# Optimization experiments

Hardware: AMD Instinct MI355X
Metric: run time of the kernel (lower is better)

The kernel has to match this reference:

```python
import jax, jax.numpy as jnp
import numpy as np

EPS = 0.05    # geomloss: blur**p with p=1, blur=0.05
NITER = 30    # fixed Sinkhorn iterations (geomloss uses eps-scaling; fixed-eps loop is the reference math)


def _cost(x, y):
    # x:(N,3), y:(M,3) -> (N,M) Euclidean distance (p=1 ground cost)
    d2 = jnp.sum((x[:, None, :] - y[None, :, :]) ** 2, axis=-1)
    return jnp.sqrt(d2 + 1e-12)


def _sinkhorn_ot(x, y):
    # Entropic OT cost between uniform measures on x (N pts) and y (M pts), log-domain Sinkhorn.
    n, m = x.shape[0], y.shape[0]
    C = _cost(x, y)                                  # (N,M)
    log_a = jnp.full((n,), -jnp.log(jnp.float32(n)), dtype=x.dtype)
    log_b = jnp.full((m,), -jnp.log(jnp.float32(m)), dtype=x.dtype)

    def step(carry, _):
        f, g = carry
        # f_i = -eps * LSE_j( log_b_j + (g_j - C_ij)/eps )
        f = -EPS * jax.nn.logsumexp(log_b[None, :] + (g[None, :] - C) / EPS, axis=1)
        g = -EPS * jax.nn.logsumexp(log_a[:, None] + (f[:, None] - C) / EPS, axis=0)
        return (f, g), None

    f0 = jnp.zeros((n,), dtype=x.dtype)
    g0 = jnp.zeros((m,), dtype=x.dtype)
    (f, g), _ = jax.lax.scan(step, (f0, g0), None, length=NITER)
    a = jnp.exp(log_a)
    b = jnp.exp(log_b)
    return jnp.sum(a * f) + jnp.sum(b * g)


def _sinkhorn_divergence(x, y):
    # Debiased Sinkhorn divergence: S(x,y) = OT(x,y) - 0.5*OT(x,x) - 0.5*OT(y,y)
    return _sinkhorn_ot(x, y) - 0.5 * _sinkhorn_ot(x, x) - 0.5 * _sinkhorn_ot(y, y)


def setup_inputs() -> dict:
    key = jax.random.key(0)
    k1, k2 = jax.random.split(key)
    B, N, M = 8, 2048, 2048
    xyz1 = jax.random.normal(k1, (B, N, 3), dtype=jnp.float32)
    xyz2 = jax.random.normal(k2, (B, M, 3), dtype=jnp.float32)
    return {"xyz1": xyz1, "xyz2": xyz2}


def reference(xyz1, xyz2):
    # Per-batch Sinkhorn divergence, averaged over batch (original loops over b; vmap is the
    # vectorized equivalent since clouds are independent).
    losses = jax.vmap(_sinkhorn_divergence)(xyz1, xyz2)   # (B,)
    return jnp.sum(losses) / xyz1.shape[0]
```

## Files before the change

kernel.cpp:

```cpp
#include <hip/hip_runtime.h>

#define NPTS    2048
#define NBATCH  8
#define NPROB   24
#define NITER   30
#define TPB     512
#define WPB     8
#define NJOBS   32
#define HCOLS   1024
#define CPW     128

constexpr float KSC = 28.853900817779268f;
constexpr float C1f = 0.38123094930796995f;
constexpr float C2f = 0.03465735902799726f;

typedef float v2f __attribute__((ext_vector_type(2)));

__device__ __forceinline__ float fexp2(float x) { return __builtin_amdgcn_exp2f(x); }
__device__ __forceinline__ float flog2(float x) { return __builtin_amdgcn_logf(x); }
__device__ __forceinline__ float fsqrt(float x) { return __builtin_amdgcn_sqrtf(x); }

__global__ __launch_bounds__(256)
void init_sums(float* __restrict__ gsum)
{
    int i = blockIdx.x * 256 + threadIdx.x;
    if (i < NPROB * 2 * NPTS) gsum[i] = 1024.0f;
}

__device__ __forceinline__ void problem_barrier(unsigned* arrive, unsigned* epoch,
                                                unsigned phase, int nbpp, int tid)
{
    __syncthreads();
    if (tid == 0) {
        unsigned old = __hip_atomic_fetch_add(arrive, 1u, __ATOMIC_ACQ_REL,
                                              __HIP_MEMORY_SCOPE_AGENT);
        if (old == (unsigned)(nbpp - 1)) {
            __hip_atomic_store(arrive, 0u, __ATOMIC_RELAXED, __HIP_MEMORY_SCOPE_AGENT);
            __hip_atomic_store(epoch, phase, __ATOMIC_RELEASE, __HIP_MEMORY_SCOPE_AGENT);
        } else {
            while (__hip_atomic_load(epoch, __ATOMIC_RELAXED,
                                     __HIP_MEMORY_SCOPE_AGENT) < phase) {
                __builtin_amdgcn_s_sleep(2);
            }
            __threadfence();
        }
    }
    __syncthreads();
}

__global__ __launch_bounds__(TPB, 6)
void sinkhorn_all(const float* __restrict__ xyz1,
                  const float* __restrict__ xyz2,
                  float* __restrict__ fsum,
                  float* __restrict__ gsum,
                  unsigned* __restrict__ bars,
                  int nbpp)
{
    __shared__ float4 shC[2][HCOLS];
    __shared__ float  shS[WPB][128];

    const int tid  = threadIdx.x;
    const int lane = tid & 63;
    const int warp = tid >> 6;
    const int p    = blockIdx.x % NPROB;
    const int lb   = blockIdx.x / NPROB;
    const int b    = p / 3;
    const int k    = p - 3 * b;

    const float* xb = xyz1 + (size_t)b * NPTS * 3;
    const float* yb = xyz2 + (size_t)b * NPTS * 3;
    float* fS = fsum + (size_t)p * 2 * NPTS;
    float* gS = gsum + (size_t)p * 2 * NPTS;
    unsigned* arrive = bars + (size_t)p * 64;
    unsigned* epoch  = bars + (size_t)p * 64 + 32;

    const float* Uf = (k == 2) ? yb : xb;
    const float* Ug = (k == 0) ? yb : ((k == 1) ? xb : yb);
    const float* Vf = (k == 1) ? xb : yb;
    const float* Vg = (k == 2) ? yb : xb;
    const int sideG = (Vg == Vf) ? 0 : 1;

    auto stage_coords = [&](const float* __restrict__ V, int side, int h) {
        if (tid < 256) {
            const float4* V4 = (const float4*)V;
            const int i0 = 3 * (h * 256 + tid);
            const float4 a  = V4[i0 + 0];
            const float4 bb = V4[i0 + 1];
            const float4 cc = V4[i0 + 2];
            const int c = 4 * tid;
            shC[side][c + 0] = make_float4(a.x,  a.y,  a.z,  0.f);
            shC[side][c + 1] = make_float4(a.w,  bb.x, bb.y, 0.f);
            shC[side][c + 2] = make_float4(bb.z, bb.w, cc.x, 0.f);
            shC[side][c + 3] = make_float4(cc.y, cc.z, cc.w, 0.f);
        }
    };
    auto stage_w = [&](const float* __restrict__ S, int side, int h) {
        const int c  = 2 * tid;
        const int gc = h * HCOLS + c;
        const float2 t0 = *(const float2*)(S + gc);
        const float2 t1 = *(const float2*)(S + NPTS + gc);
        shC[side][c + 0].w = 11.0f - flog2(t0.x + t1.x);
        shC[side][c + 1].w = 11.0f - flog2(t0.y + t1.y);
    };
    auto stage_full = [&](const float* __restrict__ V, const float* __restrict__ S,
                          int side, int h) {
        if (tid < 256) {
            const float4* V4 = (const float4*)V;
            const int i0 = 3 * (h * 256 + tid);
            const float4 a  = V4[i0 + 0];
            const float4 bb = V4[i0 + 1];
            const float4 cc = V4[i0 + 2];
            const int c  = 4 * tid;
            const int gc = h * HCOLS + c;
            const float4 t0 = *(const float4*)(S + gc);
            const float4 t1 = *(const float4*)(S + NPTS + gc);
            shC[side][c + 0] = make_float4(a.x,  a.y,  a.z,  11.0f - flog2(t0.x + t1.x));
            shC[side][c + 1] = make_float4(a.w,  bb.x, bb.y, 11.0f - flog2(t0.y + t1.y));
            shC[side][c + 2] = make_float4(bb.z, bb.w, cc.x, 11.0f - flog2(t0.z + t1.z));
            shC[side][c + 3] = make_float4(cc.y, cc.z, cc.w, 11.0f - flog2(t0.w + t1.w));
        }
    };

    auto do_pass = [&](const float* __restrict__ U, float* __restrict__ oS,
                       int side, int h, int rc) {
        __syncthreads();
        const int r0 = rc * 128 + lane, r1 = r0 + 64;
        const v2f ux = {U[3*r0],   U[3*r1]};
        const v2f uy = {U[3*r0+1], U[3*r1+1]};
        const v2f uz = {U[3*r0+2], U[3*r1+2]};
        const v2f e12 = {1e-12f, 1e-12f};
        const v2f nK  = {-KSC, -KSC};
        v2f s0 = {0.f, 0.f}, s1 = {0.f, 0.f}, s2 = {0.f, 0.f}, s3 = {0.f, 0.f};

        auto term = [&](const float4 v) -> v2f {
            v2f dx = ux - (v2f){v.x, v.x};
            v2f dy = uy - (v2f){v.y, v.y};
            v2f dz = uz - (v2f){v.z, v.z};
            v2f d2 = __builtin_elementwise_fma(dz, dz, e12);
            d2 = __builtin_elementwise_fma(dy, dy, d2);
            d2 = __builtin_elementwise_fma(dx, dx, d2);
            v2f sq  = {fsqrt(d2.x), fsqrt(d2.y)};
            v2f arg = __builtin_elementwise_fma(nK, sq, (v2f){v.w, v.w});
            return (v2f){fexp2(arg.x), fexp2(arg.y)};
        };
        const int cb = warp * CPW;
        #pragma unroll 2
        for (int c = cb; c < cb + CPW; c += 4) {
            const float4 v0 = shC[side][c + 0];
            const float4 v1 = shC[side][c + 1];
            const float4 v2 = shC[side][c + 2];
            const float4 v3 = shC[side][c + 3];
            s0 += term(v0);
            s1 += term(v1);
            s2 += term(v2);
            s3 += term(v3);
        }
        shS[warp][lane]      = (s0.x + s1.x) + (s2.x + s3.x);
        shS[warp][lane + 64] = (s0.y + s1.y) + (s2.y + s3.y);
        __syncthreads();
        if (tid < 128) {
            float t = shS[0][tid];
            #pragma unroll
            for (int w = 1; w < WPB; ++w) t += shS[w][tid];
            oS[h * NPTS + rc * 128 + tid] = t;
        }
        __syncthreads();
    };

    if (nbpp == NJOBS) {
        const int h  = lb & 1;
        const int rc = lb >> 1;
        stage_coords(Vf, 0, h);
        if (sideG == 1) stage_coords(Vg, 1, h);

        for (int it = 0; it < NITER; ++it) {
            stage_w(gS, 0, h);
            do_pass(Uf, fS, 0, h, rc);
            problem_barrier(arrive, epoch, (unsigned)(2 * it + 1), nbpp, tid);
            stage_w(fS, sideG, h);
            do_pass(Ug, gS, sideG, h, rc);
            problem_barrier(arrive, epoch, (unsigned)(2 * it + 2), nbpp, tid);
        }
    } else {
        for (int it = 0; it < NITER; ++it) {
            for (int j = lb; j < NJOBS; j += nbpp) {
                stage_full(Vf, gS, 0, j & 1);
                do_pass(Uf, fS, 0, j & 1, j >> 1);
            }
            problem_barrier(arrive, epoch, (unsigned)(2 * it + 1), nbpp, tid);
            for (int j = lb; j < NJOBS; j += nbpp) {
                stage_full(Vg, fS, 0, j & 1);
                do_pass(Ug, gS, 0, j & 1, j >> 1);
            }
            problem_barrier(arrive, epoch, (unsigned)(2 * it + 2), nbpp, tid);
        }
    }
}

__global__ __launch_bounds__(TPB, 1)
void final_reduce(const float* __restrict__ fsum, const float* __restrict__ gsum,
                  float* __restrict__ out)
{
    __shared__ double red[WPB];
    const int tid  = threadIdx.x;
    const int lane = tid & 63;
    const int warp = tid >> 6;

    double acc = 0.0;
    for (int idx = tid; idx < 2 * NPROB * NPTS; idx += TPB) {
        const bool isF = idx < NPROB * NPTS;
        const int rem  = isF ? idx : idx - NPROB * NPTS;
        const int pp   = rem >> 11;
        const int j    = rem & (NPTS - 1);
        const float* S = (isF ? fsum : gsum) + (size_t)pp * 2 * NPTS;
        const float t  = S[j] + S[NPTS + j];
        const float val = C1f - C2f * flog2(t);
        const float w   = (pp % 3 == 0) ? 1.0f : -0.5f;
        acc += (double)val * (double)w;
    }
    #pragma unroll
    for (int off = 32; off > 0; off >>= 1) acc += __shfl_xor(acc, off);
    if (lane == 0) red[warp] = acc;
    __syncthreads();
    if (warp == 0) {
        double v2 = (lane < WPB) ? red[lane] : 0.0;
        #pragma unroll
        for (int off = 32; off > 0; off >>= 1) v2 += __shfl_xor(v2, off);
        if (lane == 0) out[0] = (float)(v2 / (double)(NBATCH * NPTS));
    }
}

extern "C" void kernel_launch(void* const* d_in, const int* in_sizes, int n_in,
                              void* d_out, int out_size, void* d_ws, size_t ws_size,
                              hipStream_t stream)
{
    const float* xyz1 = (const float*)d_in[0];
    const float* xyz2 = (const float*)d_in[1];
    float* out = (float*)d_out;

    float* fsum = (float*)d_ws;
    float* gsum = fsum + (size_t)NPROB * 2 * NPTS;
    unsigned* bars = (unsigned*)(gsum + (size_t)NPROB * 2 * NPTS);

    hipMemsetAsync(bars, 0, (size_t)NPROB * 64 * sizeof(unsigned), stream);
    init_sums<<<(NPROB * 2 * NPTS + 255) / 256, 256, 0, stream>>>(gsum);

    int maxB = 0;
    hipOccupancyMaxActiveBlocksPerMultiprocessor(&maxB, sinkhorn_all, TPB, 0);
    if (maxB < 1) maxB = 1;
    int bpp = (maxB * 256) / NPROB;
    if (bpp > NJOBS) bpp = NJOBS;
    if (bpp < 1) bpp = 1;
    int nblk = NPROB * bpp;

    void* args[] = { (void*)&xyz1, (void*)&xyz2, (void*)&fsum, (void*)&gsum,
                     (void*)&bars, (void*)&bpp };
    hipLaunchCooperativeKernel((void*)sinkhorn_all, dim3(nblk), dim3(TPB),
                               args, 0, stream);

    final_reduce<<<1, TPB, 0, stream>>>(fsum, gsum, out);
}
```

Measured before the change: 2.562 ms.

## Morton-sort point clouds before Sinkhorn and interleave per-warp column assignment

Adds a prep kernel that sorts each point cloud by a 30-bit Morton code with a shared-memory bitonic sort, writes the reordered coordinates and per-64-point bounding boxes, and feeds the sorted clouds to the Sinkhorn kernel. Each warp now takes columns in an interleaved stride of 32 instead of a contiguous 128-column chunk. The bounding boxes are not used yet, apparently groundwork for later cluster-based skipping. The sort adds an extra launch and workspace, and reordering points (uniform weights) leaves the result unchanged except for floating-point summation order.

New measurement: 2.554 ms. No clear change (-0.3%).

```diff
diff --git a/kernel.cpp b/kernel.cpp
--- a/kernel.cpp
+++ b/kernel.cpp
@@ -8,7 +8,6 @@
 #define WPB     8
 #define NJOBS   32
 #define HCOLS   1024
-#define CPW     128
 
 constexpr float KSC = 28.853900817779268f;
 constexpr float C1f = 0.38123094930796995f;
@@ -19,6 +18,78 @@
 __device__ __forceinline__ float fexp2(float x) { return __builtin_amdgcn_exp2f(x); }
 __device__ __forceinline__ float flog2(float x) { return __builtin_amdgcn_logf(x); }
 __device__ __forceinline__ float fsqrt(float x) { return __builtin_amdgcn_sqrtf(x); }
+
+__device__ __forceinline__ unsigned long long mspread(unsigned v) {
+    unsigned long long x = v & 1023ull;
+    x = (x | (x << 16)) & 0x030000FFull;
+    x = (x | (x << 8))  & 0x0300F00Full;
+    x = (x | (x << 4))  & 0x030C30C3ull;
+    x = (x | (x << 2))  & 0x09249249ull;
+    return x;
+}
+__device__ __forceinline__ unsigned q10(float v) {
+    int q = (int)((v + 8.0f) * 64.0f);
+    return (unsigned)(q < 0 ? 0 : (q > 1023 ? 1023 : q));
+}
+
+__global__ __launch_bounds__(TPB)
+void prep_sort(const float* __restrict__ xyz1, const float* __restrict__ xyz2,
+               float* __restrict__ pc, float* __restrict__ bbox)
+{
+    __shared__ unsigned long long keys[NPTS];
+    const int s  = blockIdx.x;
+    const int b  = s >> 1;
+    const float* src = (s & 1) ? (xyz2 + (size_t)b * NPTS * 3)
+                               : (xyz1 + (size_t)b * NPTS * 3);
+    const int tid = threadIdx.x;
+
+    for (int i = tid; i < NPTS; i += TPB) {
+        float x = src[3*i], y = src[3*i+1], z = src[3*i+2];
+        unsigned long long code = (mspread(q10(x)) << 2) |
+                                  (mspread(q10(y)) << 1) |
+                                   mspread(q10(z));
+        keys[i] = (code << 11) | (unsigned long long)i;
+    }
+    __syncthreads();
+
+    for (int k = 2; k <= NPTS; k <<= 1) {
+        for (int j = k >> 1; j > 0; j >>= 1) {
+            for (int t = tid; t < NPTS / 2; t += TPB) {
+                const int lo = t & (j - 1);
+                const int i  = ((t - lo) << 1) + lo;
+                const int ix = i + j;
+                const bool asc = ((i & k) == 0);
+                unsigned long long a = keys[i], c = keys[ix];
+                if ((a > c) == asc) { keys[i] = c; keys[ix] = a; }
+            }
+            __syncthreads();
+        }
+    }
+
+    float* dst = pc + (size_t)s * NPTS * 3;
+    for (int i = tid; i < NPTS; i += TPB) {
+        const int pi = (int)(keys[i] & 2047ull);
+        dst[3*i+0] = src[3*pi+0];
+        dst[3*i+1] = src[3*pi+1];
+        dst[3*i+2] = src[3*pi+2];
+    }
+
+    if (tid < 32) {
+        float lox = 1e30f, loy = 1e30f, loz = 1e30f;
+        float hix = -1e30f, hiy = -1e30f, hiz = -1e30f;
+        for (int q = 0; q < 64; ++q) {
+            const int pi = (int)(keys[tid * 64 + q] & 2047ull);
+            const float x = src[3*pi], y = src[3*pi+1], z = src[3*pi+2];
+            lox = fminf(lox, x); hix = fmaxf(hix, x);
+            loy = fminf(loy, y); hiy = fmaxf(hiy, y);
+            loz = fminf(loz, z); hiz = fmaxf(hiz, z);
+        }
+        float* bb = bbox + ((size_t)s * 32 + tid) * 8;
+        bb[0] = lox; bb[1] = loy; bb[2] = loz;
+        bb[3] = hix; bb[4] = hiy; bb[5] = hiz;
+        bb[6] = 0.f; bb[7] = 0.f;
+    }
+}
 
 __global__ __launch_bounds__(256)
 void init_sums(float* __restrict__ gsum)
@@ -49,8 +120,7 @@
 }
 
 __global__ __launch_bounds__(TPB, 6)
-void sinkhorn_all(const float* __restrict__ xyz1,
-                  const float* __restrict__ xyz2,
+void sinkhorn_all(const float* __restrict__ pc,
                   float* __restrict__ fsum,
                   float* __restrict__ gsum,
                   unsigned* __restrict__ bars,
@@ -67,8 +137,8 @@
     const int b    = p / 3;
     const int k    = p - 3 * b;
 
-    const float* xb = xyz1 + (size_t)b * NPTS * 3;
-    const float* yb = xyz2 + (size_t)b * NPTS * 3;
+    const float* xb = pc + (size_t)(2 * b) * NPTS * 3;
+    const float* yb = pc + (size_t)(2 * b + 1) * NPTS * 3;
     float* fS = fsum + (size_t)p * 2 * NPTS;
     float* gS = gsum + (size_t)p * 2 * NPTS;
     unsigned* arrive = bars + (size_t)p * 64;
@@ -143,9 +213,10 @@
             v2f arg = __builtin_elementwise_fma(nK, sq, (v2f){v.w, v.w});
             return (v2f){fexp2(arg.x), fexp2(arg.y)};
         };
-        const int cb = warp * CPW;
+        const int cbase = warp * 4;
         #pragma unroll 2
-        for (int c = cb; c < cb + CPW; c += 4) {
+        for (int g = 0; g < 32; ++g) {
+            const int c = cbase + g * 32;
             const float4 v0 = shC[side][c + 0];
             const float4 v1 = shC[side][c + 1];
             const float4 v2 = shC[side][c + 2];
@@ -240,9 +311,12 @@
 
     float* fsum = (float*)d_ws;
     float* gsum = fsum + (size_t)NPROB * 2 * NPTS;
-    unsigned* bars = (unsigned*)(gsum + (size_t)NPROB * 2 * NPTS);
+    float* pc   = gsum + (size_t)NPROB * 2 * NPTS;
+    float* bbox = pc   + (size_t)16 * NPTS * 3;
+    unsigned* bars = (unsigned*)(bbox + (size_t)16 * 32 * 8);
 
     hipMemsetAsync(bars, 0, (size_t)NPROB * 64 * sizeof(unsigned), stream);
+    prep_sort<<<16, TPB, 0, stream>>>(xyz1, xyz2, pc, bbox);
     init_sums<<<(NPROB * 2 * NPTS + 255) / 256, 256, 0, stream>>>(gsum);
 
     int maxB = 0;
@@ -253,8 +327,7 @@
     if (bpp < 1) bpp = 1;
     int nblk = NPROB * bpp;
 
-    void* args[] = { (void*)&xyz1, (void*)&xyz2, (void*)&fsum, (void*)&gsum,
-                     (void*)&bars, (void*)&bpp };
+    void* args[] = { (void*)&pc, (void*)&fsum, (void*)&gsum, (void*)&bars, (void*)&bpp };
     hipLaunchCooperativeKernel((void*)sinkhorn_all, dim3(nblk), dim3(TPB),
                                args, 0, stream);
 
```
